# Optimization experiments

Measured on AMD Instinct MI355X. Metric: run time of the kernel, lower is better.

Reference implementation:

```python
import jax, jax.numpy as jnp
import numpy as np

N, D = 1024, 128
C = 1.0                 # curvature c
MIN_NORM = 1e-15
PROJ_EPS = 4e-3         # HGCN float32 projection eps


def _artanh(x):
    return jnp.arctanh(jnp.clip(x, -1.0 + 1e-7, 1.0 - 1e-7))


def _lambda_x(x, c):
    x2 = jnp.sum(x * x, axis=-1, keepdims=True)
    return 2.0 / jnp.clip(1.0 - c * x2, MIN_NORM)


def _mobius_add(x, y, c):
    x2 = jnp.sum(x * x, axis=-1, keepdims=True)
    y2 = jnp.sum(y * y, axis=-1, keepdims=True)
    xy = jnp.sum(x * y, axis=-1, keepdims=True)
    num = (1.0 + 2.0 * c * xy + c * y2) * x + (1.0 - c * x2) * y
    den = 1.0 + 2.0 * c * xy + c * c * x2 * y2
    return num / jnp.clip(den, MIN_NORM)


def _logmap0(p, c):
    sqrt_c = c ** 0.5
    pn = jnp.clip(jnp.linalg.norm(p, axis=-1, keepdims=True), MIN_NORM)
    return (_artanh(sqrt_c * pn) / (sqrt_c * pn)) * p


def _logmap(p1, p2, c):
    # log map of p2 in the tangent space at p1 (broadcasts)
    sub = _mobius_add(-p1, p2, c)
    sn = jnp.clip(jnp.linalg.norm(sub, axis=-1, keepdims=True), MIN_NORM)
    lam = _lambda_x(p1, c)
    sqrt_c = c ** 0.5
    return (2.0 / (sqrt_c * lam)) * _artanh(sqrt_c * sn) * sub / sn


def _expmap(p, u, c):
    # exp map of tangent vector u at point p
    sqrt_c = c ** 0.5
    un = jnp.clip(jnp.linalg.norm(u, axis=-1, keepdims=True), MIN_NORM)
    second = jnp.tanh(0.5 * sqrt_c * _lambda_x(p, c) * un) * u / (sqrt_c * un)
    return _mobius_add(p, second, c)


def _proj(x, c):
    n = jnp.clip(jnp.linalg.norm(x, axis=-1, keepdims=True), MIN_NORM)
    maxnorm = (1.0 - PROJ_EPS) / (c ** 0.5)
    return jnp.where(n > maxnorm, x / n * maxnorm, x)


def setup_inputs() -> dict:
    key = jax.random.key(0)
    k1, k2, k3, k4 = jax.random.split(key, 4)
    # points inside the Poincare ball (norm ~ 0.05*sqrt(D) ~ 0.57 < 1)
    x = 0.05 * jax.random.normal(k1, (N, D), dtype=jnp.float32)
    adj = jax.random.uniform(k2, (N, N), dtype=jnp.float32)
    # DenseAtt: Linear(2*D -> 1)
    att_w = jax.random.normal(k3, (2 * D,), dtype=jnp.float32) / np.sqrt(2.0 * D)
    att_b = 0.01 * jax.random.normal(k4, (), dtype=jnp.float32)
    return {"x": x, "adj": adj, "att_w": att_w, "att_b": att_b}


def reference(x, adj, att_w, att_b):
    c = C
    d = x.shape[-1]
    x_tan = _logmap0(x, c)                               # [N, d]
    # per-node local tangents: logmap_{x_i}(x_j) for all i, j -> [N, N, d]
    x_loc = _logmap(x[:, None, :], x[None, :, :], c)
    # DenseAtt: sigmoid(Linear(cat(x_i, x_j))) * adj, decomposed to avoid [N,N,2d]
    left = x_tan @ att_w[:d]                             # [N]
    right = x_tan @ att_w[d:]                            # [N]
    att = jax.nn.sigmoid(left[:, None] + right[None, :] + att_b) * adj  # [N, N]
    support_t = jnp.einsum('ij,ijd->id', att, x_loc)     # [N, d]
    return _proj(_expmap(x, support_t, c), c)
```

## Files before the change

kernel.cpp:

```cpp
#include <hip/hip_runtime.h>

#define NN 1024
#define DD 128
#define LDU 36

__device__ __forceinline__ float frcp(float x) {
  return __builtin_amdgcn_rcpf(x);
}
__device__ __forceinline__ float fsqrt(float x) {
  return __builtin_amdgcn_sqrtf(x);
}
__device__ __forceinline__ float artanh_ratio(float z) {
  z = fminf(z, 1.0f - 1e-7f);
  if (z < 1e-4f) return 1.0f + z * z * (1.0f / 3.0f);
  return 0.5f * (__logf(1.0f + z) - __logf(1.0f - z)) * frcp(z);
}
__device__ __forceinline__ float ftanh(float a) {
  const float e = __expf(-2.0f * a);
  return (1.0f - e) * frcp(1.0f + e);
}

__global__ __launch_bounds__(256) void k2_pairs(
    const float* __restrict__ x, const float* __restrict__ adj,
    const float* __restrict__ aw, const float* __restrict__ bptr,
    float* __restrict__ W, float* __restrict__ PA) {
  __shared__ __align__(16) float xiT[DD * 64];
  __shared__ __align__(16) float xjT[DD * 64];
  __shared__ float s_nx2i[64], s_lft[64], s_nx2j[64], s_rgt[64];
  const int t = threadIdx.x;
  const int bi = blockIdx.y, bj = blockIdx.x;
  const int tx = t & 15, ty = t >> 4;
  const int gi0 = bi * 64 + ty * 4;
  const int gj0 = bj * 64 + tx * 4;

  float4 ajv[4];
#pragma unroll
  for (int i = 0; i < 4; ++i) {
    ajv[i] = *(const float4*)&adj[(size_t)(gi0 + i) * NN + gj0];
  }
  const float attb = bptr[0];

  {
    const int r = t & 63;
    const int kq = t >> 6;
    const float* si = x + (bi * 64 + r) * DD + kq * 32;
    const float* sj = x + (bj * 64 + r) * DD + kq * 32;
#pragma unroll
    for (int m = 0; m < 8; ++m) {
      const int k0 = kq * 32 + m * 4;
      const float4 vi = *(const float4*)(si + m * 4);
      const float4 vj = *(const float4*)(sj + m * 4);
      xiT[(k0 + 0) * 64 + r] = vi.x;
      xiT[(k0 + 1) * 64 + r] = vi.y;
      xiT[(k0 + 2) * 64 + r] = vi.z;
      xiT[(k0 + 3) * 64 + r] = vi.w;
      xjT[(k0 + 0) * 64 + r] = vj.x;
      xjT[(k0 + 1) * 64 + r] = vj.y;
      xjT[(k0 + 2) * 64 + r] = vj.z;
      xjT[(k0 + 3) * 64 + r] = vj.w;
    }
  }
  __syncthreads();

  {
    const int r = (t >> 1) & 63;
    const int h = t & 1;
    const bool jp = (t >= 128);
    const float* panel = jp ? xjT : xiT;
    const float* wv = aw + (jp ? DD : 0);
    float sa = 0.0f, sb = 0.0f;
    const int k0 = h * 64;
#pragma unroll 8
    for (int k = 0; k < 64; ++k) {
      const float v = panel[(k0 + k) * 64 + r];
      sa = fmaf(v, v, sa);
      sb = fmaf(v, wv[k0 + k], sb);
    }
    sa += __shfl_xor(sa, 1, 64);
    sb += __shfl_xor(sb, 1, 64);
    if (h == 0) {
      const float pn = fmaxf(fsqrt(sa), 1e-15f);
      const float hh = artanh_ratio(pn);
      if (jp) { s_nx2j[r] = sa; s_rgt[r] = hh * sb; }
      else    { s_nx2i[r] = sa; s_lft[r] = hh * sb; }
    }
  }
  __syncthreads();

  float acc[4][4] = {};
#pragma unroll 2
  for (int kb = 0; kb < DD; kb += 4) {
    float4 A[4], B[4];
#pragma unroll
    for (int q = 0; q < 4; ++q) {
      A[q] = *(const float4*)&xiT[(kb + q) * 64 + ty * 4];
      B[q] = *(const float4*)&xjT[(kb + q) * 64 + tx * 4];
    }
#pragma unroll
    for (int q = 0; q < 4; ++q) {
      const float aa[4] = {A[q].x, A[q].y, A[q].z, A[q].w};
      const float bb[4] = {B[q].x, B[q].y, B[q].z, B[q].w};
#pragma unroll
      for (int i = 0; i < 4; ++i)
#pragma unroll
        for (int j = 0; j < 4; ++j) acc[i][j] = fmaf(aa[i], bb[j], acc[i][j]);
    }
  }
  float ny2v[4], rv[4];
#pragma unroll
  for (int j = 0; j < 4; ++j) {
    ny2v[j] = s_nx2j[tx * 4 + j];
    rv[j] = s_rgt[tx * 4 + j];
  }
  float sua[4];
#pragma unroll
  for (int i = 0; i < 4; ++i) {
    const float xi2 = s_nx2i[ty * 4 + i];
    const float li = s_lft[ty * 4 + i];
    const float beta = 1.0f - xi2;
    const float betac = fmaxf(beta, 1e-15f);
    const float av[4] = {ajv[i].x, ajv[i].y, ajv[i].z, ajv[i].w};
    float u4[4];
    float ua = 0.0f;
#pragma unroll
    for (int j = 0; j < 4; ++j) {
      const float s = acc[i][j];
      const float al = 1.0f - 2.0f * s + ny2v[j];
      const float den = fmaxf(1.0f - 2.0f * s + xi2 * ny2v[j], 1e-15f);
      const float rden = frcp(den);
      float s2 = fmaxf(al * al * xi2 - 2.0f * al * beta * s + beta * beta * ny2v[j], 0.0f);
      s2 = s2 * rden * rden;
      const float sn = fmaxf(fsqrt(s2), 1e-15f);
      const float G = betac * artanh_ratio(sn);
      const float sig = frcp(1.0f + __expf(-(li + rv[j] + attb)));
      const float u = sig * av[j] * G * rden;
      u4[j] = u;
      ua = fmaf(u, al, ua);
    }
    float4 st; st.x = u4[0]; st.y = u4[1]; st.z = u4[2]; st.w = u4[3];
    *(float4*)&W[(size_t)(gi0 + i) * NN + gj0] = st;
    sua[i] = ua;
  }
#pragma unroll
  for (int m = 1; m < 16; m <<= 1) {
#pragma unroll
    for (int i = 0; i < 4; ++i) sua[i] += __shfl_xor(sua[i], m, 64);
  }
  if (tx == 0) {
#pragma unroll
    for (int i = 0; i < 4; ++i) PA[(gi0 + i) * 16 + bj] = sua[i];
  }
}

__global__ __launch_bounds__(256) void k3_vpart(
    const float* __restrict__ x, const float* __restrict__ W,
    float* __restrict__ Vp) {
  __shared__ __align__(16) float uT[128 * LDU];
  __shared__ __align__(16) float xT[64 * DD];
  const int t = threadIdx.x;
  const int kt = blockIdx.x, rt = blockIdx.y;
  {
    const int r = t >> 3;
    const int c0 = (t & 7) * 16;
    const float* wrow = &W[(size_t)(rt * 32 + r) * NN + kt * 128 + c0];
#pragma unroll
    for (int m = 0; m < 4; ++m) {
      const float4 v = *(const float4*)(wrow + m * 4);
      uT[(c0 + m * 4 + 0) * LDU + r] = v.x;
      uT[(c0 + m * 4 + 1) * LDU + r] = v.y;
      uT[(c0 + m * 4 + 2) * LDU + r] = v.z;
      uT[(c0 + m * 4 + 3) * LDU + r] = v.w;
    }
  }
  const int tx = t & 31, ty = t >> 5;
  float acc[4][4] = {};
  for (int jh = 0; jh < 2; ++jh) {
    __syncthreads();
    {
      const float* xsrc = &x[(size_t)(kt * 128 + jh * 64) * DD];
#pragma unroll
      for (int p = 0; p < 8; ++p) {
        *(float4*)&xT[p * 1024 + t * 4] = *(const float4*)&xsrc[p * 1024 + t * 4];
      }
    }
    __syncthreads();
#pragma unroll 2
    for (int kb = 0; kb < 64; kb += 4) {
      float4 A[4], B[4];
#pragma unroll
      for (int q = 0; q < 4; ++q) {
        A[q] = *(const float4*)&uT[(jh * 64 + kb + q) * LDU + ty * 4];
        B[q] = *(const float4*)&xT[(kb + q) * DD + tx * 4];
      }
#pragma unroll
      for (int q = 0; q < 4; ++q) {
        const float aa[4] = {A[q].x, A[q].y, A[q].z, A[q].w};
        const float bb[4] = {B[q].x, B[q].y, B[q].z, B[q].w};
#pragma unroll
        for (int i = 0; i < 4; ++i)
#pragma unroll
          for (int j = 0; j < 4; ++j) acc[i][j] = fmaf(aa[i], bb[j], acc[i][j]);
      }
    }
  }
  const int row0 = rt * 32 + ty * 4;
#pragma unroll
  for (int i = 0; i < 4; ++i) {
    float4 s; s.x = acc[i][0]; s.y = acc[i][1]; s.z = acc[i][2]; s.w = acc[i][3];
    *(float4*)&Vp[((size_t)kt * NN + row0 + i) * DD + tx * 4] = s;
  }
}

__global__ __launch_bounds__(256) void k4_final(
    const float* __restrict__ x, const float* __restrict__ Vp,
    const float* __restrict__ PA, float* __restrict__ out) {
  const int t = threadIdx.x;
  const int w = t >> 6;
  const int l = t & 63;
  const int row = blockIdx.x * 4 + w;

  const float2 xv = *(const float2*)&x[row * DD + 2 * l];
  const float xi0 = xv.x, xi1 = xv.y;
  float ra = xi0 * xi0 + xi1 * xi1;
#pragma unroll
  for (int m = 1; m < 64; m <<= 1) ra += __shfl_xor(ra, m, 64);
  const float nx2i = ra;

  float v0 = 0.0f, v1 = 0.0f;
#pragma unroll
  for (int kt = 0; kt < 8; ++kt) {
    const float2 vv = *(const float2*)&Vp[((size_t)kt * NN + row) * DD + 2 * l];
    v0 += vv.x;
    v1 += vv.y;
  }
  float sa = (l < 16) ? PA[row * 16 + l] : 0.0f;
#pragma unroll
  for (int m = 1; m < 64; m <<= 1) sa += __shfl_xor(sa, m, 64);

  const float beta = 1.0f - nx2i;
  const float betac = fmaxf(beta, 1e-15f);
  const float u0 = beta * v0 - sa * xi0;
  const float u1 = beta * v1 - sa * xi1;
  float p0 = u0 * u0 + u1 * u1;
  float p1 = xi0 * u0 + xi1 * u1;
#pragma unroll
  for (int m = 1; m < 64; m <<= 1) {
    p0 += __shfl_xor(p0, m, 64);
    p1 += __shfl_xor(p1, m, 64);
  }
  const float un = fmaxf(fsqrt(p0), 1e-15f);
  const float tau = ftanh(frcp(betac) * un) * frcp(un);
  const float y2 = tau * tau * p0;
  const float xy = tau * p1;
  const float numx = 1.0f + 2.0f * xy + y2;
  const float dene = fmaxf(1.0f + 2.0f * xy + nx2i * y2, 1e-15f);
  const float rdene = frcp(dene);
  float r0 = (numx * xi0 + beta * tau * u0) * rdene;
  float r1 = (numx * xi1 + beta * tau * u1) * rdene;
  const float n2 = fmaxf(numx * numx * nx2i + 2.0f * numx * beta * xy + beta * beta * y2, 0.0f);
  const float n = fmaxf(fsqrt(n2) * rdene, 1e-15f);
  const float maxn = 1.0f - 4e-3f;
  if (n > maxn) {
    const float sc = maxn * frcp(n);
    r0 *= sc;
    r1 *= sc;
  }
  float2 ro; ro.x = r0; ro.y = r1;
  *(float2*)&out[row * DD + 2 * l] = ro;
}

__global__ __launch_bounds__(256) void hypagg_fused(
    const float* __restrict__ x, const float* __restrict__ adj,
    const float* __restrict__ aw, const float* __restrict__ bptr,
    float* __restrict__ out) {
  __shared__ __align__(16) float xi_lds[4 * DD];
  __shared__ __align__(16) float w2_lds[DD];
  const int t = threadIdx.x;
  const int w = t >> 6;
  const int l = t & 63;
  const int row = blockIdx.x * 4 + w;

  xi_lds[t] = x[blockIdx.x * 4 * DD + t];
  xi_lds[t + 256] = x[blockIdx.x * 4 * DD + t + 256];
  if (t < DD) w2_lds[t] = aw[DD + t];
  __syncthreads();

  const float attb = bptr[0];
  const float* xi = &xi_lds[w * DD];
  const float xi0 = xi[l];
  const float xi1 = xi[l + 64];

  float ra = xi0 * xi0 + xi1 * xi1;
  float rb = xi0 * aw[l] + xi1 * aw[l + 64];
#pragma unroll
  for (int m = 1; m < 64; m <<= 1) {
    ra += __shfl_xor(ra, m, 64);
    rb += __shfl_xor(rb, m, 64);
  }
  const float nx2i = ra;
  const float beta = 1.0f - nx2i;
  const float betac = fmaxf(beta, 1e-15f);
  const float hi = artanh_ratio(fmaxf(fsqrt(nx2i), 1e-15f));
  const float lfti = hi * rb;

  float V0 = 0.0f, V1 = 0.0f, SA = 0.0f;

  for (int j0 = 0; j0 < NN; j0 += 64) {
    const int jj = j0 + l;
    const float* xj = x + jj * DD;
    float s = 0.0f, ny2 = 0.0f, rj = 0.0f;
#pragma unroll 8
    for (int k4 = 0; k4 < DD / 4; ++k4) {
      const float4 b4 = *(const float4*)(xj + k4 * 4);
      const float4 a4 = *(const float4*)(xi + k4 * 4);
      const float4 w4 = *(const float4*)(&w2_lds[k4 * 4]);
      s   = fmaf(a4.x, b4.x, fmaf(a4.y, b4.y, fmaf(a4.z, b4.z, fmaf(a4.w, b4.w, s))));
      ny2 = fmaf(b4.x, b4.x, fmaf(b4.y, b4.y, fmaf(b4.z, b4.z, fmaf(b4.w, b4.w, ny2))));
      rj  = fmaf(w4.x, b4.x, fmaf(w4.y, b4.y, fmaf(w4.z, b4.z, fmaf(w4.w, b4.w, rj))));
    }
    const float hj = artanh_ratio(fmaxf(fsqrt(ny2), 1e-15f));
    const float rgtj = hj * rj;
    const float al = 1.0f - 2.0f * s + ny2;
    const float den = fmaxf(1.0f - 2.0f * s + nx2i * ny2, 1e-15f);
    const float rden = frcp(den);
    float s2 = fmaxf(al * al * nx2i - 2.0f * al * beta * s + beta * beta * ny2, 0.0f);
    s2 = s2 * rden * rden;
    const float sn = fmaxf(fsqrt(s2), 1e-15f);
    const float G = betac * artanh_ratio(sn);
    const float sig = frcp(1.0f + __expf(-(lfti + rgtj + attb)));
    const float u = sig * adj[row * NN + jj] * G * rden;
    SA = fmaf(u, al, SA);
#pragma unroll 16
    for (int jq = 0; jq < 64; ++jq) {
      const float uq = __shfl(u, jq, 64);
      const float xd0 = x[(j0 + jq) * DD + l];
      const float xd1 = x[(j0 + jq) * DD + l + 64];
      V0 = fmaf(uq, xd0, V0);
      V1 = fmaf(uq, xd1, V1);
    }
  }

#pragma unroll
  for (int m = 1; m < 64; m <<= 1) SA += __shfl_xor(SA, m, 64);

  const float u0 = beta * V0 - SA * xi0;
  const float u1 = beta * V1 - SA * xi1;
  float p0 = u0 * u0 + u1 * u1;
  float p1 = xi0 * u0 + xi1 * u1;
#pragma unroll
  for (int m = 1; m < 64; m <<= 1) {
    p0 += __shfl_xor(p0, m, 64);
    p1 += __shfl_xor(p1, m, 64);
  }
  const float un = fmaxf(fsqrt(p0), 1e-15f);
  const float tau = ftanh(frcp(betac) * un) * frcp(un);
  const float y2 = tau * tau * p0;
  const float xy = tau * p1;
  const float numx = 1.0f + 2.0f * xy + y2;
  const float dene = fmaxf(1.0f + 2.0f * xy + nx2i * y2, 1e-15f);
  const float rdene = frcp(dene);
  float r0 = (numx * xi0 + beta * tau * u0) * rdene;
  float r1 = (numx * xi1 + beta * tau * u1) * rdene;
  const float n2 = fmaxf(numx * numx * nx2i + 2.0f * numx * beta * xy + beta * beta * y2, 0.0f);
  const float n = fmaxf(fsqrt(n2) * rdene, 1e-15f);
  const float maxn = 1.0f - 4e-3f;
  if (n > maxn) {
    const float sc = maxn * frcp(n);
    r0 *= sc;
    r1 *= sc;
  }
  out[row * DD + l] = r0;
  out[row * DD + l + 64] = r1;
}

extern "C" void kernel_launch(void* const* d_in, const int* in_sizes, int n_in,
                              void* d_out, int out_size, void* d_ws, size_t ws_size,
                              hipStream_t stream) {
  const float* x = nullptr;
  const float* adj = nullptr;
  const float* aw = nullptr;
  const float* ab = nullptr;
  for (int i = 0; i < n_in; ++i) {
    switch (in_sizes[i]) {
      case NN * DD:  x   = (const float*)d_in[i]; break;
      case NN * NN:  adj = (const float*)d_in[i]; break;
      case 2 * DD:   aw  = (const float*)d_in[i]; break;
      case 1:        ab  = (const float*)d_in[i]; break;
      default: break;
    }
  }
  float* out = (float*)d_out;

  const size_t need = ((size_t)NN * NN + 8 * (size_t)NN * DD + NN * 16) * sizeof(float);
  if (ws_size >= need) {
    float* W  = (float*)d_ws;
    float* Vp = W + (size_t)NN * NN;
    float* PA = Vp + 8 * (size_t)NN * DD;
    hipLaunchKernelGGL(k2_pairs, dim3(16, 16), dim3(256), 0, stream,
                       x, adj, aw, ab, W, PA);
    hipLaunchKernelGGL(k3_vpart, dim3(8, 32), dim3(256), 0, stream, x, W, Vp);
    hipLaunchKernelGGL(k4_final, dim3(NN / 4), dim3(256), 0, stream,
                       x, Vp, PA, out);
  } else {
    hipLaunchKernelGGL(hypagg_fused, dim3(NN / 4), dim3(256), 0, stream,
                       x, adj, aw, ab, out);
  }
}
```

Before: 29.73 us.

## Fuse partial aggregation and finalisation into one per-row-block kernel

Merges the tiled W·x partial-product kernel and the final expmap/projection kernel into a single kernel. Each block owns 4 output rows and walks all 1024 neighbours, staging 64-row chunks of x in double-buffered LDS, broadcasting W entries via wave shuffles, then reducing the per-wave partials in LDS. This removes the 8-way Vp partial buffer, its global write and read-back, and one kernel launch. In exchange, every block re-reads the whole of x from cache, and the inner loop is shuffle-heavy and has less register reuse than the old 4x4 outer-product tile.

After: 42.65 us. 1.43x slower.

```diff
diff --git a/kernel.cpp b/kernel.cpp
--- a/kernel.cpp
+++ b/kernel.cpp
@@ -2,7 +2,6 @@
 
 #define NN 1024
 #define DD 128
-#define LDU 36
 
 __device__ __forceinline__ float frcp(float x) {
   return __builtin_amdgcn_rcpf(x);
@@ -152,91 +151,73 @@
   }
 }
 
-__global__ __launch_bounds__(256) void k3_vpart(
+__global__ __launch_bounds__(256) void k34_agg(
     const float* __restrict__ x, const float* __restrict__ W,
-    float* __restrict__ Vp) {
-  __shared__ __align__(16) float uT[128 * LDU];
-  __shared__ __align__(16) float xT[64 * DD];
+    const float* __restrict__ PA, float* __restrict__ out) {
+  __shared__ __align__(16) float xT[2][64 * DD];
+  __shared__ float vred[4][4][DD];
   const int t = threadIdx.x;
-  const int kt = blockIdx.x, rt = blockIdx.y;
-  {
-    const int r = t >> 3;
-    const int c0 = (t & 7) * 16;
-    const float* wrow = &W[(size_t)(rt * 32 + r) * NN + kt * 128 + c0];
-#pragma unroll
-    for (int m = 0; m < 4; ++m) {
-      const float4 v = *(const float4*)(wrow + m * 4);
-      uT[(c0 + m * 4 + 0) * LDU + r] = v.x;
-      uT[(c0 + m * 4 + 1) * LDU + r] = v.y;
-      uT[(c0 + m * 4 + 2) * LDU + r] = v.z;
-      uT[(c0 + m * 4 + 3) * LDU + r] = v.w;
-    }
-  }
-  const int tx = t & 31, ty = t >> 5;
-  float acc[4][4] = {};
-  for (int jh = 0; jh < 2; ++jh) {
+  const int w = t >> 6, l = t & 63;
+  const int r0 = blockIdx.x * 4;
+  const int lr = l >> 4, lc = l & 15;
+
+#pragma unroll
+  for (int p = 0; p < 8; ++p)
+    *(float4*)&xT[0][p * 1024 + t * 4] = *(const float4*)&x[p * 1024 + t * 4];
+  __syncthreads();
+
+  float V0[4] = {0.0f, 0.0f, 0.0f, 0.0f};
+  float V1[4] = {0.0f, 0.0f, 0.0f, 0.0f};
+
+  for (int c = 0; c < 16; ++c) {
+    const float wl = W[(size_t)(r0 + lr) * NN + c * 64 + w * 16 + lc];
+    if (c < 15) {
+      const float* xsrc = &x[(size_t)(c + 1) * 64 * DD];
+#pragma unroll
+      for (int p = 0; p < 8; ++p)
+        *(float4*)&xT[(c + 1) & 1][p * 1024 + t * 4] =
+            *(const float4*)&xsrc[p * 1024 + t * 4];
+    }
+    const float* xb = xT[c & 1];
+#pragma unroll
+    for (int jq = 0; jq < 16; ++jq) {
+      const int j = w * 16 + jq;
+      const float xv0 = xb[j * DD + l];
+      const float xv1 = xb[j * DD + l + 64];
+      const float u0 = __shfl(wl, 0 * 16 + jq, 64);
+      const float u1 = __shfl(wl, 1 * 16 + jq, 64);
+      const float u2 = __shfl(wl, 2 * 16 + jq, 64);
+      const float u3 = __shfl(wl, 3 * 16 + jq, 64);
+      V0[0] = fmaf(u0, xv0, V0[0]); V1[0] = fmaf(u0, xv1, V1[0]);
+      V0[1] = fmaf(u1, xv0, V0[1]); V1[1] = fmaf(u1, xv1, V1[1]);
+      V0[2] = fmaf(u2, xv0, V0[2]); V1[2] = fmaf(u2, xv1, V1[2]);
+      V0[3] = fmaf(u3, xv0, V0[3]); V1[3] = fmaf(u3, xv1, V1[3]);
+    }
     __syncthreads();
-    {
-      const float* xsrc = &x[(size_t)(kt * 128 + jh * 64) * DD];
-#pragma unroll
-      for (int p = 0; p < 8; ++p) {
-        *(float4*)&xT[p * 1024 + t * 4] = *(const float4*)&xsrc[p * 1024 + t * 4];
-      }
-    }
-    __syncthreads();
-#pragma unroll 2
-    for (int kb = 0; kb < 64; kb += 4) {
-      float4 A[4], B[4];
-#pragma unroll
-      for (int q = 0; q < 4; ++q) {
-        A[q] = *(const float4*)&uT[(jh * 64 + kb + q) * LDU + ty * 4];
-        B[q] = *(const float4*)&xT[(kb + q) * DD + tx * 4];
-      }
-#pragma unroll
-      for (int q = 0; q < 4; ++q) {
-        const float aa[4] = {A[q].x, A[q].y, A[q].z, A[q].w};
-        const float bb[4] = {B[q].x, B[q].y, B[q].z, B[q].w};
-#pragma unroll
-        for (int i = 0; i < 4; ++i)
-#pragma unroll
-          for (int j = 0; j < 4; ++j) acc[i][j] = fmaf(aa[i], bb[j], acc[i][j]);
-      }
-    }
-  }
-  const int row0 = rt * 32 + ty * 4;
-#pragma unroll
-  for (int i = 0; i < 4; ++i) {
-    float4 s; s.x = acc[i][0]; s.y = acc[i][1]; s.z = acc[i][2]; s.w = acc[i][3];
-    *(float4*)&Vp[((size_t)kt * NN + row0 + i) * DD + tx * 4] = s;
-  }
-}
-
-__global__ __launch_bounds__(256) void k4_final(
-    const float* __restrict__ x, const float* __restrict__ Vp,
-    const float* __restrict__ PA, float* __restrict__ out) {
-  const int t = threadIdx.x;
-  const int w = t >> 6;
-  const int l = t & 63;
-  const int row = blockIdx.x * 4 + w;
-
-  const float2 xv = *(const float2*)&x[row * DD + 2 * l];
-  const float xi0 = xv.x, xi1 = xv.y;
+  }
+
+#pragma unroll
+  for (int r = 0; r < 4; ++r) {
+    vred[w][r][l] = V0[r];
+    vred[w][r][l + 64] = V1[r];
+  }
+  __syncthreads();
+
+  const int row = r0 + w;
+  float v0 = vred[0][w][l] + vred[1][w][l] + vred[2][w][l] + vred[3][w][l];
+  float v1 = vred[0][w][l + 64] + vred[1][w][l + 64] +
+             vred[2][w][l + 64] + vred[3][w][l + 64];
+
+  float sa = (l < 16) ? PA[row * 16 + l] : 0.0f;
+#pragma unroll
+  for (int m = 1; m < 64; m <<= 1) sa += __shfl_xor(sa, m, 64);
+
+  const float xi0 = x[row * DD + l];
+  const float xi1 = x[row * DD + l + 64];
   float ra = xi0 * xi0 + xi1 * xi1;
 #pragma unroll
   for (int m = 1; m < 64; m <<= 1) ra += __shfl_xor(ra, m, 64);
   const float nx2i = ra;
-
-  float v0 = 0.0f, v1 = 0.0f;
-#pragma unroll
-  for (int kt = 0; kt < 8; ++kt) {
-    const float2 vv = *(const float2*)&Vp[((size_t)kt * NN + row) * DD + 2 * l];
-    v0 += vv.x;
-    v1 += vv.y;
-  }
-  float sa = (l < 16) ? PA[row * 16 + l] : 0.0f;
-#pragma unroll
-  for (int m = 1; m < 64; m <<= 1) sa += __shfl_xor(sa, m, 64);
-
   const float beta = 1.0f - nx2i;
   const float betac = fmaxf(beta, 1e-15f);
   const float u0 = beta * v0 - sa * xi0;
@@ -255,18 +236,18 @@
   const float numx = 1.0f + 2.0f * xy + y2;
   const float dene = fmaxf(1.0f + 2.0f * xy + nx2i * y2, 1e-15f);
   const float rdene = frcp(dene);
-  float r0 = (numx * xi0 + beta * tau * u0) * rdene;
-  float r1 = (numx * xi1 + beta * tau * u1) * rdene;
+  float r0o = (numx * xi0 + beta * tau * u0) * rdene;
+  float r1o = (numx * xi1 + beta * tau * u1) * rdene;
   const float n2 = fmaxf(numx * numx * nx2i + 2.0f * numx * beta * xy + beta * beta * y2, 0.0f);
   const float n = fmaxf(fsqrt(n2) * rdene, 1e-15f);
   const float maxn = 1.0f - 4e-3f;
   if (n > maxn) {
     const float sc = maxn * frcp(n);
-    r0 *= sc;
-    r1 *= sc;
-  }
-  float2 ro; ro.x = r0; ro.y = r1;
-  *(float2*)&out[row * DD + 2 * l] = ro;
+    r0o *= sc;
+    r1o *= sc;
+  }
+  out[row * DD + l] = r0o;
+  out[row * DD + l + 64] = r1o;
 }
 
 __global__ __launch_bounds__(256) void hypagg_fused(
@@ -391,16 +372,14 @@
   }
   float* out = (float*)d_out;
 
-  const size_t need = ((size_t)NN * NN + 8 * (size_t)NN * DD + NN * 16) * sizeof(float);
+  const size_t need = ((size_t)NN * NN + NN * 16) * sizeof(float);
   if (ws_size >= need) {
     float* W  = (float*)d_ws;
-    float* Vp = W + (size_t)NN * NN;
-    float* PA = Vp + 8 * (size_t)NN * DD;
+    float* PA = W + (size_t)NN * NN;
     hipLaunchKernelGGL(k2_pairs, dim3(16, 16), dim3(256), 0, stream,
                        x, adj, aw, ab, W, PA);
-    hipLaunchKernelGGL(k3_vpart, dim3(8, 32), dim3(256), 0, stream, x, W, Vp);
-    hipLaunchKernelGGL(k4_final, dim3(NN / 4), dim3(256), 0, stream,
-                       x, Vp, PA, out);
+    hipLaunchKernelGGL(k34_agg, dim3(NN / 4), dim3(256), 0, stream,
+                       x, W, PA, out);
   } else {
     hipLaunchKernelGGL(hypagg_fused, dim3(NN / 4), dim3(256), 0, stream,
                        x, adj, aw, ab, out);
```

## Fuse three kernels into one persistent kernel with atomic grid barriers

Applied to the files above, without the earlier changes.

Merges the pair-weight, partial matrix-product and final expmap kernels into one 256-block kernel that reuses a shared LDS arena and separates phases with a global atomic-counter barrier. A memset resets the counter before each launch. This removes two kernel launch gaps and their tail effects, at the cost of spin-waiting and the assumption that all 256 blocks are co-resident, which could deadlock if they are not.

Result: slower. 69.79 us (+134.7%).

```diff
diff --git a/kernel.cpp b/kernel.cpp
--- a/kernel.cpp
+++ b/kernel.cpp
@@ -20,177 +20,88 @@
   return (1.0f - e) * frcp(1.0f + e);
 }
 
-__global__ __launch_bounds__(256) void k2_pairs(
+__global__ __launch_bounds__(256) void mega(
     const float* __restrict__ x, const float* __restrict__ adj,
     const float* __restrict__ aw, const float* __restrict__ bptr,
-    float* __restrict__ W, float* __restrict__ PA) {
-  __shared__ __align__(16) float xiT[DD * 64];
-  __shared__ __align__(16) float xjT[DD * 64];
-  __shared__ float s_nx2i[64], s_lft[64], s_nx2j[64], s_rgt[64];
+    float* __restrict__ W, float* __restrict__ Vp, float* __restrict__ PA,
+    unsigned* __restrict__ cnt, float* __restrict__ out) {
+  __shared__ __align__(16) float arena[16640];
   const int t = threadIdx.x;
-  const int bi = blockIdx.y, bj = blockIdx.x;
-  const int tx = t & 15, ty = t >> 4;
-  const int gi0 = bi * 64 + ty * 4;
-  const int gj0 = bj * 64 + tx * 4;
-
-  float4 ajv[4];
-#pragma unroll
-  for (int i = 0; i < 4; ++i) {
-    ajv[i] = *(const float4*)&adj[(size_t)(gi0 + i) * NN + gj0];
-  }
-  const float attb = bptr[0];
+  const int blk = blockIdx.x;
 
   {
-    const int r = t & 63;
-    const int kq = t >> 6;
-    const float* si = x + (bi * 64 + r) * DD + kq * 32;
-    const float* sj = x + (bj * 64 + r) * DD + kq * 32;
-#pragma unroll
-    for (int m = 0; m < 8; ++m) {
-      const int k0 = kq * 32 + m * 4;
-      const float4 vi = *(const float4*)(si + m * 4);
-      const float4 vj = *(const float4*)(sj + m * 4);
-      xiT[(k0 + 0) * 64 + r] = vi.x;
-      xiT[(k0 + 1) * 64 + r] = vi.y;
-      xiT[(k0 + 2) * 64 + r] = vi.z;
-      xiT[(k0 + 3) * 64 + r] = vi.w;
-      xjT[(k0 + 0) * 64 + r] = vj.x;
-      xjT[(k0 + 1) * 64 + r] = vj.y;
-      xjT[(k0 + 2) * 64 + r] = vj.z;
-      xjT[(k0 + 3) * 64 + r] = vj.w;
-    }
-  }
-  __syncthreads();
-
-  {
-    const int r = (t >> 1) & 63;
-    const int h = t & 1;
-    const bool jp = (t >= 128);
-    const float* panel = jp ? xjT : xiT;
-    const float* wv = aw + (jp ? DD : 0);
-    float sa = 0.0f, sb = 0.0f;
-    const int k0 = h * 64;
+    float* xiT = arena;
+    float* xjT = arena + 8192;
+    float* s_nx2i = arena + 16384;
+    float* s_lft = arena + 16448;
+    float* s_nx2j = arena + 16512;
+    float* s_rgt = arena + 16576;
+    const int bi = blk >> 4, bj = blk & 15;
+    const int tx = t & 15, ty = t >> 4;
+    const int gi0 = bi * 64 + ty * 4;
+    const int gj0 = bj * 64 + tx * 4;
+
+    float4 ajv[4];
+#pragma unroll
+    for (int i = 0; i < 4; ++i)
+      ajv[i] = *(const float4*)&adj[(size_t)(gi0 + i) * NN + gj0];
+    const float attb = bptr[0];
+
+    {
+      const int r = t & 63;
+      const int kq = t >> 6;
+      const float* si = x + (bi * 64 + r) * DD + kq * 32;
+      const float* sj = x + (bj * 64 + r) * DD + kq * 32;
+#pragma unroll
+      for (int m = 0; m < 8; ++m) {
+        const int k0 = kq * 32 + m * 4;
+        const float4 vi = *(const float4*)(si + m * 4);
+        const float4 vj = *(const float4*)(sj + m * 4);
+        xiT[(k0 + 0) * 64 + r] = vi.x;
+        xiT[(k0 + 1) * 64 + r] = vi.y;
+        xiT[(k0 + 2) * 64 + r] = vi.z;
+        xiT[(k0 + 3) * 64 + r] = vi.w;
+        xjT[(k0 + 0) * 64 + r] = vj.x;
+        xjT[(k0 + 1) * 64 + r] = vj.y;
+        xjT[(k0 + 2) * 64 + r] = vj.z;
+        xjT[(k0 + 3) * 64 + r] = vj.w;
+      }
+    }
+    __syncthreads();
+
+    {
+      const int r = (t >> 1) & 63;
+      const int h = t & 1;
+      const bool jp = (t >= 128);
+      const float* panel = jp ? xjT : xiT;
+      const float* wv = aw + (jp ? DD : 0);
+      float sa = 0.0f, sb = 0.0f;
+      const int k0 = h * 64;
 #pragma unroll 8
-    for (int k = 0; k < 64; ++k) {
-      const float v = panel[(k0 + k) * 64 + r];
-      sa = fmaf(v, v, sa);
-      sb = fmaf(v, wv[k0 + k], sb);
-    }
-    sa += __shfl_xor(sa, 1, 64);
-    sb += __shfl_xor(sb, 1, 64);
-    if (h == 0) {
-      const float pn = fmaxf(fsqrt(sa), 1e-15f);
-      const float hh = artanh_ratio(pn);
-      if (jp) { s_nx2j[r] = sa; s_rgt[r] = hh * sb; }
-      else    { s_nx2i[r] = sa; s_lft[r] = hh * sb; }
-    }
-  }
-  __syncthreads();
-
-  float acc[4][4] = {};
+      for (int k = 0; k < 64; ++k) {
+        const float v = panel[(k0 + k) * 64 + r];
+        sa = fmaf(v, v, sa);
+        sb = fmaf(v, wv[k0 + k], sb);
+      }
+      sa += __shfl_xor(sa, 1, 64);
+      sb += __shfl_xor(sb, 1, 64);
+      if (h == 0) {
+        const float pn = fmaxf(fsqrt(sa), 1e-15f);
+        const float hh = artanh_ratio(pn);
+        if (jp) { s_nx2j[r] = sa; s_rgt[r] = hh * sb; }
+        else    { s_nx2i[r] = sa; s_lft[r] = hh * sb; }
+      }
+    }
+    __syncthreads();
+
+    float acc[4][4] = {};
 #pragma unroll 2
-  for (int kb = 0; kb < DD; kb += 4) {
-    float4 A[4], B[4];
-#pragma unroll
-    for (int q = 0; q < 4; ++q) {
-      A[q] = *(const float4*)&xiT[(kb + q) * 64 + ty * 4];
-      B[q] = *(const float4*)&xjT[(kb + q) * 64 + tx * 4];
-    }
-#pragma unroll
-    for (int q = 0; q < 4; ++q) {
-      const float aa[4] = {A[q].x, A[q].y, A[q].z, A[q].w};
-      const float bb[4] = {B[q].x, B[q].y, B[q].z, B[q].w};
-#pragma unroll
-      for (int i = 0; i < 4; ++i)
-#pragma unroll
-        for (int j = 0; j < 4; ++j) acc[i][j] = fmaf(aa[i], bb[j], acc[i][j]);
-    }
-  }
-  float ny2v[4], rv[4];
-#pragma unroll
-  for (int j = 0; j < 4; ++j) {
-    ny2v[j] = s_nx2j[tx * 4 + j];
-    rv[j] = s_rgt[tx * 4 + j];
-  }
-  float sua[4];
-#pragma unroll
-  for (int i = 0; i < 4; ++i) {
-    const float xi2 = s_nx2i[ty * 4 + i];
-    const float li = s_lft[ty * 4 + i];
-    const float beta = 1.0f - xi2;
-    const float betac = fmaxf(beta, 1e-15f);
-    const float av[4] = {ajv[i].x, ajv[i].y, ajv[i].z, ajv[i].w};
-    float u4[4];
-    float ua = 0.0f;
-#pragma unroll
-    for (int j = 0; j < 4; ++j) {
-      const float s = acc[i][j];
-      const float al = 1.0f - 2.0f * s + ny2v[j];
-      const float den = fmaxf(1.0f - 2.0f * s + xi2 * ny2v[j], 1e-15f);
-      const float rden = frcp(den);
-      float s2 = fmaxf(al * al * xi2 - 2.0f * al * beta * s + beta * beta * ny2v[j], 0.0f);
-      s2 = s2 * rden * rden;
-      const float sn = fmaxf(fsqrt(s2), 1e-15f);
-      const float G = betac * artanh_ratio(sn);
-      const float sig = frcp(1.0f + __expf(-(li + rv[j] + attb)));
-      const float u = sig * av[j] * G * rden;
-      u4[j] = u;
-      ua = fmaf(u, al, ua);
-    }
-    float4 st; st.x = u4[0]; st.y = u4[1]; st.z = u4[2]; st.w = u4[3];
-    *(float4*)&W[(size_t)(gi0 + i) * NN + gj0] = st;
-    sua[i] = ua;
-  }
-#pragma unroll
-  for (int m = 1; m < 16; m <<= 1) {
-#pragma unroll
-    for (int i = 0; i < 4; ++i) sua[i] += __shfl_xor(sua[i], m, 64);
-  }
-  if (tx == 0) {
-#pragma unroll
-    for (int i = 0; i < 4; ++i) PA[(gi0 + i) * 16 + bj] = sua[i];
-  }
-}
-
-__global__ __launch_bounds__(256) void k3_vpart(
-    const float* __restrict__ x, const float* __restrict__ W,
-    float* __restrict__ Vp) {
-  __shared__ __align__(16) float uT[128 * LDU];
-  __shared__ __align__(16) float xT[64 * DD];
-  const int t = threadIdx.x;
-  const int kt = blockIdx.x, rt = blockIdx.y;
-  {
-    const int r = t >> 3;
-    const int c0 = (t & 7) * 16;
-    const float* wrow = &W[(size_t)(rt * 32 + r) * NN + kt * 128 + c0];
-#pragma unroll
-    for (int m = 0; m < 4; ++m) {
-      const float4 v = *(const float4*)(wrow + m * 4);
-      uT[(c0 + m * 4 + 0) * LDU + r] = v.x;
-      uT[(c0 + m * 4 + 1) * LDU + r] = v.y;
-      uT[(c0 + m * 4 + 2) * LDU + r] = v.z;
-      uT[(c0 + m * 4 + 3) * LDU + r] = v.w;
-    }
-  }
-  const int tx = t & 31, ty = t >> 5;
-  float acc[4][4] = {};
-  for (int jh = 0; jh < 2; ++jh) {
-    __syncthreads();
-    {
-      const float* xsrc = &x[(size_t)(kt * 128 + jh * 64) * DD];
-#pragma unroll
-      for (int p = 0; p < 8; ++p) {
-        *(float4*)&xT[p * 1024 + t * 4] = *(const float4*)&xsrc[p * 1024 + t * 4];
-      }
-    }
-    __syncthreads();
-#pragma unroll 2
-    for (int kb = 0; kb < 64; kb += 4) {
+    for (int kb = 0; kb < DD; kb += 4) {
       float4 A[4], B[4];
 #pragma unroll
       for (int q = 0; q < 4; ++q) {
-        A[q] = *(const float4*)&uT[(jh * 64 + kb + q) * LDU + ty * 4];
-        B[q] = *(const float4*)&xT[(kb + q) * DD + tx * 4];
+        A[q] = *(const float4*)&xiT[(kb + q) * 64 + ty * 4];
+        B[q] = *(const float4*)&xjT[(kb + q) * 64 + tx * 4];
       }
 #pragma unroll
       for (int q = 0; q < 4; ++q) {
@@ -202,71 +113,178 @@
           for (int j = 0; j < 4; ++j) acc[i][j] = fmaf(aa[i], bb[j], acc[i][j]);
       }
     }
-  }
-  const int row0 = rt * 32 + ty * 4;
-#pragma unroll
-  for (int i = 0; i < 4; ++i) {
-    float4 s; s.x = acc[i][0]; s.y = acc[i][1]; s.z = acc[i][2]; s.w = acc[i][3];
-    *(float4*)&Vp[((size_t)kt * NN + row0 + i) * DD + tx * 4] = s;
-  }
-}
-
-__global__ __launch_bounds__(256) void k4_final(
-    const float* __restrict__ x, const float* __restrict__ Vp,
-    const float* __restrict__ PA, float* __restrict__ out) {
-  const int t = threadIdx.x;
-  const int w = t >> 6;
-  const int l = t & 63;
-  const int row = blockIdx.x * 4 + w;
-
-  const float2 xv = *(const float2*)&x[row * DD + 2 * l];
-  const float xi0 = xv.x, xi1 = xv.y;
-  float ra = xi0 * xi0 + xi1 * xi1;
-#pragma unroll
-  for (int m = 1; m < 64; m <<= 1) ra += __shfl_xor(ra, m, 64);
-  const float nx2i = ra;
-
-  float v0 = 0.0f, v1 = 0.0f;
-#pragma unroll
-  for (int kt = 0; kt < 8; ++kt) {
-    const float2 vv = *(const float2*)&Vp[((size_t)kt * NN + row) * DD + 2 * l];
-    v0 += vv.x;
-    v1 += vv.y;
-  }
-  float sa = (l < 16) ? PA[row * 16 + l] : 0.0f;
-#pragma unroll
-  for (int m = 1; m < 64; m <<= 1) sa += __shfl_xor(sa, m, 64);
-
-  const float beta = 1.0f - nx2i;
-  const float betac = fmaxf(beta, 1e-15f);
-  const float u0 = beta * v0 - sa * xi0;
-  const float u1 = beta * v1 - sa * xi1;
-  float p0 = u0 * u0 + u1 * u1;
-  float p1 = xi0 * u0 + xi1 * u1;
-#pragma unroll
-  for (int m = 1; m < 64; m <<= 1) {
-    p0 += __shfl_xor(p0, m, 64);
-    p1 += __shfl_xor(p1, m, 64);
-  }
-  const float un = fmaxf(fsqrt(p0), 1e-15f);
-  const float tau = ftanh(frcp(betac) * un) * frcp(un);
-  const float y2 = tau * tau * p0;
-  const float xy = tau * p1;
-  const float numx = 1.0f + 2.0f * xy + y2;
-  const float dene = fmaxf(1.0f + 2.0f * xy + nx2i * y2, 1e-15f);
-  const float rdene = frcp(dene);
-  float r0 = (numx * xi0 + beta * tau * u0) * rdene;
-  float r1 = (numx * xi1 + beta * tau * u1) * rdene;
-  const float n2 = fmaxf(numx * numx * nx2i + 2.0f * numx * beta * xy + beta * beta * y2, 0.0f);
-  const float n = fmaxf(fsqrt(n2) * rdene, 1e-15f);
-  const float maxn = 1.0f - 4e-3f;
-  if (n > maxn) {
-    const float sc = maxn * frcp(n);
-    r0 *= sc;
-    r1 *= sc;
-  }
-  float2 ro; ro.x = r0; ro.y = r1;
-  *(float2*)&out[row * DD + 2 * l] = ro;
+    float ny2v[4], rv[4];
+#pragma unroll
+    for (int j = 0; j < 4; ++j) {
+      ny2v[j] = s_nx2j[tx * 4 + j];
+      rv[j] = s_rgt[tx * 4 + j];
+    }
+    float sua[4];
+#pragma unroll
+    for (int i = 0; i < 4; ++i) {
+      const float xi2 = s_nx2i[ty * 4 + i];
+      const float li = s_lft[ty * 4 + i];
+      const float beta = 1.0f - xi2;
+      const float betac = fmaxf(beta, 1e-15f);
+      const float av[4] = {ajv[i].x, ajv[i].y, ajv[i].z, ajv[i].w};
+      float u4[4];
+      float ua = 0.0f;
+#pragma unroll
+      for (int j = 0; j < 4; ++j) {
+        const float s = acc[i][j];
+        const float al = 1.0f - 2.0f * s + ny2v[j];
+        const float den = fmaxf(1.0f - 2.0f * s + xi2 * ny2v[j], 1e-15f);
+        const float rden = frcp(den);
+        float s2 = fmaxf(al * al * xi2 - 2.0f * al * beta * s + beta * beta * ny2v[j], 0.0f);
+        s2 = s2 * rden * rden;
+        const float sn = fmaxf(fsqrt(s2), 1e-15f);
+        const float G = betac * artanh_ratio(sn);
+        const float sig = frcp(1.0f + __expf(-(li + rv[j] + attb)));
+        const float u = sig * av[j] * G * rden;
+        u4[j] = u;
+        ua = fmaf(u, al, ua);
+      }
+      float4 st; st.x = u4[0]; st.y = u4[1]; st.z = u4[2]; st.w = u4[3];
+      *(float4*)&W[(size_t)(gi0 + i) * NN + gj0] = st;
+      sua[i] = ua;
+    }
+#pragma unroll
+    for (int m = 1; m < 16; m <<= 1) {
+#pragma unroll
+      for (int i = 0; i < 4; ++i) sua[i] += __shfl_xor(sua[i], m, 64);
+    }
+    if (tx == 0) {
+#pragma unroll
+      for (int i = 0; i < 4; ++i) PA[(gi0 + i) * 16 + bj] = sua[i];
+    }
+  }
+
+  __syncthreads();
+  if (t == 0) {
+    __threadfence();
+    atomicAdd(cnt, 1u);
+    while (atomicAdd(cnt, 0u) < 256u) __builtin_amdgcn_s_sleep(8);
+  }
+  __syncthreads();
+
+  {
+    float* uT = arena;
+    float* xT = arena + 4608;
+    const int kt = blk & 7, rt = blk >> 3;
+    {
+      const int r = t >> 3;
+      const int c0 = (t & 7) * 16;
+      const float* wrow = &W[(size_t)(rt * 32 + r) * NN + kt * 128 + c0];
+#pragma unroll
+      for (int m = 0; m < 4; ++m) {
+        const float4 v = *(const float4*)(wrow + m * 4);
+        uT[(c0 + m * 4 + 0) * LDU + r] = v.x;
+        uT[(c0 + m * 4 + 1) * LDU + r] = v.y;
+        uT[(c0 + m * 4 + 2) * LDU + r] = v.z;
+        uT[(c0 + m * 4 + 3) * LDU + r] = v.w;
+      }
+    }
+    const int tx = t & 31, ty = t >> 5;
+    float acc[4][4] = {};
+    for (int jh = 0; jh < 2; ++jh) {
+      __syncthreads();
+      {
+        const float* xsrc = &x[(size_t)(kt * 128 + jh * 64) * DD];
+#pragma unroll
+        for (int p = 0; p < 8; ++p) {
+          *(float4*)&xT[p * 1024 + t * 4] = *(const float4*)&xsrc[p * 1024 + t * 4];
+        }
+      }
+      __syncthreads();
+#pragma unroll 2
+      for (int kb = 0; kb < 64; kb += 4) {
+        float4 A[4], B[4];
+#pragma unroll
+        for (int q = 0; q < 4; ++q) {
+          A[q] = *(const float4*)&uT[(jh * 64 + kb + q) * LDU + ty * 4];
+          B[q] = *(const float4*)&xT[(kb + q) * DD + tx * 4];
+        }
+#pragma unroll
+        for (int q = 0; q < 4; ++q) {
+          const float aa[4] = {A[q].x, A[q].y, A[q].z, A[q].w};
+          const float bb[4] = {B[q].x, B[q].y, B[q].z, B[q].w};
+#pragma unroll
+          for (int i = 0; i < 4; ++i)
+#pragma unroll
+            for (int j = 0; j < 4; ++j) acc[i][j] = fmaf(aa[i], bb[j], acc[i][j]);
+        }
+      }
+    }
+    const int row0 = rt * 32 + ty * 4;
+#pragma unroll
+    for (int i = 0; i < 4; ++i) {
+      float4 s; s.x = acc[i][0]; s.y = acc[i][1]; s.z = acc[i][2]; s.w = acc[i][3];
+      *(float4*)&Vp[((size_t)kt * NN + row0 + i) * DD + tx * 4] = s;
+    }
+  }
+
+  __syncthreads();
+  if (t == 0) {
+    __threadfence();
+    atomicAdd(cnt, 1u);
+    while (atomicAdd(cnt, 0u) < 512u) __builtin_amdgcn_s_sleep(8);
+  }
+  __syncthreads();
+
+  {
+    const int w = t >> 6;
+    const int l = t & 63;
+    const int row = blk * 4 + w;
+
+    const float2 xv = *(const float2*)&x[row * DD + 2 * l];
+    const float xi0 = xv.x, xi1 = xv.y;
+    float ra = xi0 * xi0 + xi1 * xi1;
+#pragma unroll
+    for (int m = 1; m < 64; m <<= 1) ra += __shfl_xor(ra, m, 64);
+    const float nx2i = ra;
+
+    float v0 = 0.0f, v1 = 0.0f;
+#pragma unroll
+    for (int kt = 0; kt < 8; ++kt) {
+      const float2 vv = *(const float2*)&Vp[((size_t)kt * NN + row) * DD + 2 * l];
+      v0 += vv.x;
+      v1 += vv.y;
+    }
+    float sa = (l < 16) ? PA[row * 16 + l] : 0.0f;
+#pragma unroll
+    for (int m = 1; m < 64; m <<= 1) sa += __shfl_xor(sa, m, 64);
+
+    const float beta = 1.0f - nx2i;
+    const float betac = fmaxf(beta, 1e-15f);
+    const float u0 = beta * v0 - sa * xi0;
+    const float u1 = beta * v1 - sa * xi1;
+    float p0 = u0 * u0 + u1 * u1;
+    float p1 = xi0 * u0 + xi1 * u1;
+#pragma unroll
+    for (int m = 1; m < 64; m <<= 1) {
+      p0 += __shfl_xor(p0, m, 64);
+      p1 += __shfl_xor(p1, m, 64);
+    }
+    const float un = fmaxf(fsqrt(p0), 1e-15f);
+    const float tau = ftanh(frcp(betac) * un) * frcp(un);
+    const float y2 = tau * tau * p0;
+    const float xy = tau * p1;
+    const float numx = 1.0f + 2.0f * xy + y2;
+    const float dene = fmaxf(1.0f + 2.0f * xy + nx2i * y2, 1e-15f);
+    const float rdene = frcp(dene);
+    float r0 = (numx * xi0 + beta * tau * u0) * rdene;
+    float r1 = (numx * xi1 + beta * tau * u1) * rdene;
+    const float n2 = fmaxf(numx * numx * nx2i + 2.0f * numx * beta * xy + beta * beta * y2, 0.0f);
+    const float n = fmaxf(fsqrt(n2) * rdene, 1e-15f);
+    const float maxn = 1.0f - 4e-3f;
+    if (n > maxn) {
+      const float sc = maxn * frcp(n);
+      r0 *= sc;
+      r1 *= sc;
+    }
+    float2 ro; ro.x = r0; ro.y = r1;
+    *(float2*)&out[row * DD + 2 * l] = ro;
+  }
 }
 
 __global__ __launch_bounds__(256) void hypagg_fused(
@@ -391,16 +409,15 @@
   }
   float* out = (float*)d_out;
 
-  const size_t need = ((size_t)NN * NN + 8 * (size_t)NN * DD + NN * 16) * sizeof(float);
+  const size_t need = ((size_t)NN * NN + 8 * (size_t)NN * DD + NN * 16) * sizeof(float) + sizeof(unsigned);
   if (ws_size >= need) {
     float* W  = (float*)d_ws;
     float* Vp = W + (size_t)NN * NN;
     float* PA = Vp + 8 * (size_t)NN * DD;
-    hipLaunchKernelGGL(k2_pairs, dim3(16, 16), dim3(256), 0, stream,
-                       x, adj, aw, ab, W, PA);
-    hipLaunchKernelGGL(k3_vpart, dim3(8, 32), dim3(256), 0, stream, x, W, Vp);
-    hipLaunchKernelGGL(k4_final, dim3(NN / 4), dim3(256), 0, stream,
-                       x, Vp, PA, out);
+    unsigned* cnt = (unsigned*)(PA + NN * 16);
+    hipMemsetAsync((void*)cnt, 0, sizeof(unsigned), stream);
+    hipLaunchKernelGGL(mega, dim3(256), dim3(256), 0, stream,
+                       x, adj, aw, ab, W, Vp, PA, cnt, out);
   } else {
     hipLaunchKernelGGL(hypagg_fused, dim3(NN / 4), dim3(256), 0, stream,
                        x, adj, aw, ab, out);
```

## Fuse pair-weight kernel with U·X partial product, drop W round-trip

Applied to the files above, without the earlier changes.

The pairwise weight kernel now keeps its 64x64 tile of weights in LDS and immediately multiplies it by the corresponding 64 rows of x, writing 16 partial V slices per row instead of the full NxN weight matrix. The separate vpart kernel and the 4 MB W write/read are removed, and the final kernel now sums 16 partials instead of 8. This saves a launch and global traffic but adds more partial-sum traffic and a non-LDS x read pattern inside the fused kernel.

Result: faster. 28.21 us (-5.1%).

```diff
diff --git a/kernel.cpp b/kernel.cpp
--- a/kernel.cpp
+++ b/kernel.cpp
@@ -2,7 +2,6 @@
 
 #define NN 1024
 #define DD 128
-#define LDU 36
 
 __device__ __forceinline__ float frcp(float x) {
   return __builtin_amdgcn_rcpf(x);
@@ -20,10 +19,10 @@
   return (1.0f - e) * frcp(1.0f + e);
 }
 
-__global__ __launch_bounds__(256) void k2_pairs(
+__global__ __launch_bounds__(256) void k23_pairs_v(
     const float* __restrict__ x, const float* __restrict__ adj,
     const float* __restrict__ aw, const float* __restrict__ bptr,
-    float* __restrict__ W, float* __restrict__ PA) {
+    float* __restrict__ Vp, float* __restrict__ PA) {
   __shared__ __align__(16) float xiT[DD * 64];
   __shared__ __align__(16) float xjT[DD * 64];
   __shared__ float s_nx2i[64], s_lft[64], s_nx2j[64], s_rgt[64];
@@ -35,9 +34,8 @@
 
   float4 ajv[4];
 #pragma unroll
-  for (int i = 0; i < 4; ++i) {
+  for (int i = 0; i < 4; ++i)
     ajv[i] = *(const float4*)&adj[(size_t)(gi0 + i) * NN + gj0];
-  }
   const float attb = bptr[0];
 
   {
@@ -106,12 +104,14 @@
         for (int j = 0; j < 4; ++j) acc[i][j] = fmaf(aa[i], bb[j], acc[i][j]);
     }
   }
+
   float ny2v[4], rv[4];
 #pragma unroll
   for (int j = 0; j < 4; ++j) {
     ny2v[j] = s_nx2j[tx * 4 + j];
     rv[j] = s_rgt[tx * 4 + j];
   }
+  float4 ureg[4];
   float sua[4];
 #pragma unroll
   for (int i = 0; i < 4; ++i) {
@@ -137,8 +137,7 @@
       u4[j] = u;
       ua = fmaf(u, al, ua);
     }
-    float4 st; st.x = u4[0]; st.y = u4[1]; st.z = u4[2]; st.w = u4[3];
-    *(float4*)&W[(size_t)(gi0 + i) * NN + gj0] = st;
+    ureg[i].x = u4[0]; ureg[i].y = u4[1]; ureg[i].z = u4[2]; ureg[i].w = u4[3];
     sua[i] = ua;
   }
 #pragma unroll
@@ -150,64 +149,42 @@
 #pragma unroll
     for (int i = 0; i < 4; ++i) PA[(gi0 + i) * 16 + bj] = sua[i];
   }
-}
-
-__global__ __launch_bounds__(256) void k3_vpart(
-    const float* __restrict__ x, const float* __restrict__ W,
-    float* __restrict__ Vp) {
-  __shared__ __align__(16) float uT[128 * LDU];
-  __shared__ __align__(16) float xT[64 * DD];
-  const int t = threadIdx.x;
-  const int kt = blockIdx.x, rt = blockIdx.y;
+
+  __syncthreads();
+  float* u_lds = xiT;
+#pragma unroll
+  for (int i = 0; i < 4; ++i)
+    *(float4*)&u_lds[(ty * 4 + i) * 64 + tx * 4] = ureg[i];
+  __syncthreads();
+
   {
-    const int r = t >> 3;
-    const int c0 = (t & 7) * 16;
-    const float* wrow = &W[(size_t)(rt * 32 + r) * NN + kt * 128 + c0];
-#pragma unroll
-    for (int m = 0; m < 4; ++m) {
-      const float4 v = *(const float4*)(wrow + m * 4);
-      uT[(c0 + m * 4 + 0) * LDU + r] = v.x;
-      uT[(c0 + m * 4 + 1) * LDU + r] = v.y;
-      uT[(c0 + m * 4 + 2) * LDU + r] = v.z;
-      uT[(c0 + m * 4 + 3) * LDU + r] = v.w;
-    }
-  }
-  const int tx = t & 31, ty = t >> 5;
-  float acc[4][4] = {};
-  for (int jh = 0; jh < 2; ++jh) {
-    __syncthreads();
-    {
-      const float* xsrc = &x[(size_t)(kt * 128 + jh * 64) * DD];
-#pragma unroll
-      for (int p = 0; p < 8; ++p) {
-        *(float4*)&xT[p * 1024 + t * 4] = *(const float4*)&xsrc[p * 1024 + t * 4];
+    const int tx2 = t & 31, ty2 = t >> 5;
+    const int i0 = ty2 * 8, d0 = tx2 * 4;
+    float4 a8[8];
+#pragma unroll
+    for (int ii = 0; ii < 8; ++ii) a8[ii] = make_float4(0.0f, 0.0f, 0.0f, 0.0f);
+#pragma unroll 4
+    for (int jb = 0; jb < 16; ++jb) {
+      const int j0 = jb * 4;
+      float4 xv[4];
+#pragma unroll
+      for (int jj = 0; jj < 4; ++jj)
+        xv[jj] = *(const float4*)&x[(size_t)(bj * 64 + j0 + jj) * DD + d0];
+      float4 uv[8];
+#pragma unroll
+      for (int ii = 0; ii < 8; ++ii)
+        uv[ii] = *(const float4*)&u_lds[(i0 + ii) * 64 + j0];
+#pragma unroll
+      for (int ii = 0; ii < 8; ++ii) {
+        a8[ii].x = fmaf(uv[ii].x, xv[0].x, fmaf(uv[ii].y, xv[1].x, fmaf(uv[ii].z, xv[2].x, fmaf(uv[ii].w, xv[3].x, a8[ii].x))));
+        a8[ii].y = fmaf(uv[ii].x, xv[0].y, fmaf(uv[ii].y, xv[1].y, fmaf(uv[ii].z, xv[2].y, fmaf(uv[ii].w, xv[3].y, a8[ii].y))));
+        a8[ii].z = fmaf(uv[ii].x, xv[0].z, fmaf(uv[ii].y, xv[1].z, fmaf(uv[ii].z, xv[2].z, fmaf(uv[ii].w, xv[3].z, a8[ii].z))));
+        a8[ii].w = fmaf(uv[ii].x, xv[0].w, fmaf(uv[ii].y, xv[1].w, fmaf(uv[ii].z, xv[2].w, fmaf(uv[ii].w, xv[3].w, a8[ii].w))));
       }
     }
-    __syncthreads();
-#pragma unroll 2
-    for (int kb = 0; kb < 64; kb += 4) {
-      float4 A[4], B[4];
-#pragma unroll
-      for (int q = 0; q < 4; ++q) {
-        A[q] = *(const float4*)&uT[(jh * 64 + kb + q) * LDU + ty * 4];
-        B[q] = *(const float4*)&xT[(kb + q) * DD + tx * 4];
-      }
-#pragma unroll
-      for (int q = 0; q < 4; ++q) {
-        const float aa[4] = {A[q].x, A[q].y, A[q].z, A[q].w};
-        const float bb[4] = {B[q].x, B[q].y, B[q].z, B[q].w};
-#pragma unroll
-        for (int i = 0; i < 4; ++i)
-#pragma unroll
-          for (int j = 0; j < 4; ++j) acc[i][j] = fmaf(aa[i], bb[j], acc[i][j]);
-      }
-    }
-  }
-  const int row0 = rt * 32 + ty * 4;
-#pragma unroll
-  for (int i = 0; i < 4; ++i) {
-    float4 s; s.x = acc[i][0]; s.y = acc[i][1]; s.z = acc[i][2]; s.w = acc[i][3];
-    *(float4*)&Vp[((size_t)kt * NN + row0 + i) * DD + tx * 4] = s;
+#pragma unroll
+    for (int ii = 0; ii < 8; ++ii)
+      *(float4*)&Vp[((size_t)bj * NN + bi * 64 + i0 + ii) * DD + d0] = a8[ii];
   }
 }
 
@@ -228,7 +205,7 @@
 
   float v0 = 0.0f, v1 = 0.0f;
 #pragma unroll
-  for (int kt = 0; kt < 8; ++kt) {
+  for (int kt = 0; kt < 16; ++kt) {
     const float2 vv = *(const float2*)&Vp[((size_t)kt * NN + row) * DD + 2 * l];
     v0 += vv.x;
     v1 += vv.y;
@@ -391,14 +368,12 @@
   }
   float* out = (float*)d_out;
 
-  const size_t need = ((size_t)NN * NN + 8 * (size_t)NN * DD + NN * 16) * sizeof(float);
+  const size_t need = (16 * (size_t)NN * DD + NN * 16) * sizeof(float);
   if (ws_size >= need) {
-    float* W  = (float*)d_ws;
-    float* Vp = W + (size_t)NN * NN;
-    float* PA = Vp + 8 * (size_t)NN * DD;
-    hipLaunchKernelGGL(k2_pairs, dim3(16, 16), dim3(256), 0, stream,
-                       x, adj, aw, ab, W, PA);
-    hipLaunchKernelGGL(k3_vpart, dim3(8, 32), dim3(256), 0, stream, x, W, Vp);
+    float* Vp = (float*)d_ws;
+    float* PA = Vp + 16 * (size_t)NN * DD;
+    hipLaunchKernelGGL(k23_pairs_v, dim3(16, 16), dim3(256), 0, stream,
+                       x, adj, aw, ab, Vp, PA);
     hipLaunchKernelGGL(k4_final, dim3(NN / 4), dim3(256), 0, stream,
                        x, Vp, PA, out);
   } else {
```
